# Performance work log

Hardware: AMD Instinct MI355X
Metric: run time of the kernel (lower is better)

Reference implementation:

```python
import jax, jax.numpy as jnp
import numpy as np

V, D, A = 100000, 128, 64
L, N, K = 3, 20000, 16


def setup_inputs() -> dict:
    key = jax.random.key(0)
    k1, k2, k3, k4, k5, k6 = jax.random.split(key, 6)
    Leaf_emb = jax.random.normal(k1, (V, D), dtype=jnp.float32)
    nodes = jax.random.randint(k2, (L, N), 0, V, dtype=jnp.int32)
    neighbors = jax.random.randint(k3, (L, N, K), 0, V, dtype=jnp.int32)
    masks = jnp.zeros((L, N, K), dtype=jnp.float32)  # additive mask, 0 = valid
    weights = jax.random.normal(k4, (L, N, K), dtype=jnp.float32)
    W_att = jax.random.uniform(k5, (2 * D, A), dtype=jnp.float32)
    b_att = jnp.zeros((A,), dtype=jnp.float32)
    v_att = jax.random.uniform(k6, (A,), dtype=jnp.float32)
    return {"Leaf_emb": Leaf_emb, "nodes": nodes, "neighbors": neighbors,
            "masks": masks, "weights": weights,
            "W_att": W_att, "b_att": b_att, "v_att": v_att}


def reference(Leaf_emb, nodes, neighbors, masks, weights, W_att, b_att, v_att):
    # Sequential over L tree levels (fixed, small): each level gathers node and
    # neighbor embeddings, scores neighbors with a 2-layer attention MLP,
    # combines masked-softmax attention with softmax'd structural weights,
    # sums neighbor embeddings and scatters the result back into W_tmp.
    W_tmp = Leaf_emb
    n_levels = nodes.shape[0]
    for i in range(n_levels):
        node = nodes[i]                      # [N] (constant across K in original)
        neighbor = neighbors[i]              # [N, K]
        mask = masks[i]                      # [N, K] additive
        weight = weights[i]                  # [N, K]
        node_tmp = Leaf_emb[node][:, None, :]          # [N, 1, D] from ORIGINAL emb
        neighbor_tmp = W_tmp[neighbor]                 # [N, K, D] from running emb
        node_b = jnp.broadcast_to(node_tmp, neighbor_tmp.shape)
        att_in = jnp.concatenate([node_b, neighbor_tmp], axis=2)  # [N, K, 2D]
        mlp = jax.nn.leaky_relu(att_in @ W_att + b_att, 0.01)     # [N, K, A]
        pre = mlp @ v_att                                         # [N, K]
        att = jax.nn.softmax(pre + mask, axis=1) * jax.nn.softmax(weight, axis=1)
        temp_emb = jnp.einsum('nkd,nk->nd', neighbor_tmp, att)    # [N, D]
        W_tmp = W_tmp.at[node].set(temp_emb)
    return W_tmp
```

## Files before the change

### kernel.cpp

```cpp
#include <hip/hip_runtime.h>
#include <math.h>

#define V 100000
#define D 128
#define A 64
#define LVLS 3
#define NN 20000
#define KK 16
#define BK2 16
#define AST2 18
#define BST2 68
#define PSTRIDE 128

__global__ __launch_bounds__(256, 4)
void projall_kernel(const float* __restrict__ Leaf, const float* __restrict__ Watt,
                    const float* __restrict__ batt, float* __restrict__ projAll,
                    float* __restrict__ outp) {
    __shared__ float As[128 * AST2];
    __shared__ float Bs[BK2 * BST2];
    int t = threadIdx.x;
    int tx = t & 15, ty = t >> 4;
    int r0 = blockIdx.x * 128;
    int half = blockIdx.y;
    const float* Wmat = Watt + (size_t)half * D * A;

    int ar = t >> 2;
    int ak = (t & 3) << 2;
    const float* asrc[2];
    int arow[2];
#pragma unroll
    for (int jj = 0; jj < 2; ++jj) {
        int r = r0 + ar + 64 * jj;
        arow[jj] = r;
        int rr = r < V ? r : V - 1;
        asrc[jj] = Leaf + (size_t)rr * D + ak;
    }
    int bk = t >> 4;
    int bc = (t & 15) << 2;

    float4 bv = make_float4(0.f, 0.f, 0.f, 0.f);
    if (half == 0) bv = *(const float4*)(batt + 4 * tx);
    float acc[8][4];
#pragma unroll
    for (int i = 0; i < 8; ++i) {
        acc[i][0] = bv.x; acc[i][1] = bv.y; acc[i][2] = bv.z; acc[i][3] = bv.w;
    }

    float4 pa0 = *(const float4*)(asrc[0]);
    float4 pa1 = *(const float4*)(asrc[1]);
    float4 pb  = *(const float4*)(Wmat + (size_t)bk * A + bc);

    for (int k0 = 0; k0 < D; k0 += BK2) {
        if (k0) __syncthreads();
        *(float4*)&As[(ar +  0) * AST2 + ak] = pa0;
        *(float4*)&As[(ar + 64) * AST2 + ak] = pa1;
        *(float4*)&Bs[bk * BST2 + bc] = pb;
        if (half == 0) {
            if (arow[0] < V) *(float4*)(outp + (size_t)arow[0] * D + k0 + ak) = pa0;
            if (arow[1] < V) *(float4*)(outp + (size_t)arow[1] * D + k0 + ak) = pa1;
        }
        __syncthreads();
        int kn = k0 + BK2;
        if (kn < D) {
            pa0 = *(const float4*)(asrc[0] + kn);
            pa1 = *(const float4*)(asrc[1] + kn);
            pb  = *(const float4*)(Wmat + (size_t)(kn + bk) * A + bc);
        }
#pragma unroll
        for (int kc = 0; kc < BK2; kc += 4) {
            float4 b0 = *(const float4*)&Bs[(kc + 0) * BST2 + 4 * tx];
            float4 b1 = *(const float4*)&Bs[(kc + 1) * BST2 + 4 * tx];
            float4 b2 = *(const float4*)&Bs[(kc + 2) * BST2 + 4 * tx];
            float4 b3 = *(const float4*)&Bs[(kc + 3) * BST2 + 4 * tx];
#pragma unroll
            for (int i = 0; i < 8; ++i) {
                float4 a = *(const float4*)&As[(8 * ty + i) * AST2 + kc];
                acc[i][0] = fmaf(a.x, b0.x, acc[i][0]);
                acc[i][0] = fmaf(a.y, b1.x, acc[i][0]);
                acc[i][0] = fmaf(a.z, b2.x, acc[i][0]);
                acc[i][0] = fmaf(a.w, b3.x, acc[i][0]);
                acc[i][1] = fmaf(a.x, b0.y, acc[i][1]);
                acc[i][1] = fmaf(a.y, b1.y, acc[i][1]);
                acc[i][1] = fmaf(a.z, b2.y, acc[i][1]);
                acc[i][1] = fmaf(a.w, b3.y, acc[i][1]);
                acc[i][2] = fmaf(a.x, b0.z, acc[i][2]);
                acc[i][2] = fmaf(a.y, b1.z, acc[i][2]);
                acc[i][2] = fmaf(a.z, b2.z, acc[i][2]);
                acc[i][2] = fmaf(a.w, b3.z, acc[i][2]);
                acc[i][3] = fmaf(a.x, b0.w, acc[i][3]);
                acc[i][3] = fmaf(a.y, b1.w, acc[i][3]);
                acc[i][3] = fmaf(a.z, b2.w, acc[i][3]);
                acc[i][3] = fmaf(a.w, b3.w, acc[i][3]);
            }
        }
    }

#pragma unroll
    for (int i = 0; i < 8; ++i) {
        int gr = r0 + 8 * ty + i;
        if (gr < V) {
            float4 o = make_float4(acc[i][0], acc[i][1], acc[i][2], acc[i][3]);
            *(float4*)(projAll + (size_t)gr * PSTRIDE + half * 64 + 4 * tx) = o;
        }
    }
}

__global__ __launch_bounds__(256, 4)
void commit_kernel(const float* __restrict__ tmp, const float* __restrict__ Wmat,
                   const int* __restrict__ nodes_l, const int* __restrict__ claim,
                   float* __restrict__ outp, float* __restrict__ projAll, int do_proj) {
    __shared__ float As[64 * AST2];
    __shared__ float Bs[BK2 * BST2];
    int t = threadIdx.x;
    int tx = t & 15, ty = t >> 4;
    int r0 = blockIdx.x * 64;

    int ar = t >> 2;
    int ak = (t & 3) << 2;
    int r = r0 + ar;
    int rr = r < NN ? r : NN - 1;
    const float* asrc = tmp + (size_t)rr * D + ak;
    int vrow = nodes_l[rr];
    int win = (r < NN) && (claim[vrow] == rr);

    int bk = t >> 4;
    int bc = (t & 15) << 2;

    float acc[4][4];
#pragma unroll
    for (int i = 0; i < 4; ++i) {
        acc[i][0] = 0.f; acc[i][1] = 0.f; acc[i][2] = 0.f; acc[i][3] = 0.f;
    }

    float4 pa = *(const float4*)(asrc);
    float4 pb = make_float4(0.f, 0.f, 0.f, 0.f);
    if (do_proj) pb = *(const float4*)(Wmat + (size_t)bk * A + bc);

    for (int k0 = 0; k0 < D; k0 += BK2) {
        if (k0) __syncthreads();
        *(float4*)&As[ar * AST2 + ak] = pa;
        if (do_proj) *(float4*)&Bs[bk * BST2 + bc] = pb;
        if (win)
            *(float4*)(outp + (size_t)vrow * D + k0 + ak) = pa;
        __syncthreads();
        int kn = k0 + BK2;
        if (kn < D) {
            pa = *(const float4*)(asrc + kn);
            if (do_proj) pb = *(const float4*)(Wmat + (size_t)(kn + bk) * A + bc);
        }
        if (do_proj) {
#pragma unroll
            for (int kc = 0; kc < BK2; kc += 4) {
                float4 b0 = *(const float4*)&Bs[(kc + 0) * BST2 + 4 * tx];
                float4 b1 = *(const float4*)&Bs[(kc + 1) * BST2 + 4 * tx];
                float4 b2 = *(const float4*)&Bs[(kc + 2) * BST2 + 4 * tx];
                float4 b3 = *(const float4*)&Bs[(kc + 3) * BST2 + 4 * tx];
#pragma unroll
                for (int i = 0; i < 4; ++i) {
                    float4 a = *(const float4*)&As[(4 * ty + i) * AST2 + kc];
                    acc[i][0] = fmaf(a.x, b0.x, acc[i][0]);
                    acc[i][0] = fmaf(a.y, b1.x, acc[i][0]);
                    acc[i][0] = fmaf(a.z, b2.x, acc[i][0]);
                    acc[i][0] = fmaf(a.w, b3.x, acc[i][0]);
                    acc[i][1] = fmaf(a.x, b0.y, acc[i][1]);
                    acc[i][1] = fmaf(a.y, b1.y, acc[i][1]);
                    acc[i][1] = fmaf(a.z, b2.y, acc[i][1]);
                    acc[i][1] = fmaf(a.w, b3.y, acc[i][1]);
                    acc[i][2] = fmaf(a.x, b0.z, acc[i][2]);
                    acc[i][2] = fmaf(a.y, b1.z, acc[i][2]);
                    acc[i][2] = fmaf(a.z, b2.z, acc[i][2]);
                    acc[i][2] = fmaf(a.w, b3.z, acc[i][2]);
                    acc[i][3] = fmaf(a.x, b0.w, acc[i][3]);
                    acc[i][3] = fmaf(a.y, b1.w, acc[i][3]);
                    acc[i][3] = fmaf(a.z, b2.w, acc[i][3]);
                    acc[i][3] = fmaf(a.w, b3.w, acc[i][3]);
                }
            }
        }
    }

    if (do_proj) {
#pragma unroll
        for (int i = 0; i < 4; ++i) {
            int gr = r0 + 4 * ty + i;
            if (gr < NN) {
                int v = nodes_l[gr];
                if (claim[v] == gr) {
                    float4 o = make_float4(acc[i][0], acc[i][1], acc[i][2], acc[i][3]);
                    *(float4*)(projAll + (size_t)v * PSTRIDE + 64 + 4 * tx) = o;
                }
            }
        }
    }
}

__global__ __launch_bounds__(256)
void attn_kernel(const float* __restrict__ Wc, const float* __restrict__ projAll,
                 const int* __restrict__ nodes_l, const int* __restrict__ neigh,
                 const float* __restrict__ maskp, const float* __restrict__ weightp,
                 const float* __restrict__ v_att, float* __restrict__ tmp) {
    int lane = threadIdx.x & 63;
    int n = blockIdx.x * 4 + (threadIdx.x >> 6);
    int k16 = lane & 15, q = lane >> 4;

    int   vnode = nodes_l[n];
    int   nbk = neigh[n * KK + k16];
    float wv  = weightp[n * KK + k16];
    float mk  = maskp[n * KK + k16];

    const float* npr = projAll + (size_t)vnode * PSTRIDE + q * 16;
    const float* var = v_att + q * 16;
    const float* pr  = projAll + (size_t)nbk * PSTRIDE + 64 + q * 16;

    float part = 0.f;
#pragma unroll
    for (int j = 0; j < 16; j += 4) {
        float4 npv = *(const float4*)(npr + j);
        float4 vav = *(const float4*)(var + j);
        float4 pv  = *(const float4*)(pr + j);
        float x;
        x = npv.x + pv.x; x = fmaxf(x, 0.01f * x); part = fmaf(x, vav.x, part);
        x = npv.y + pv.y; x = fmaxf(x, 0.01f * x); part = fmaf(x, vav.y, part);
        x = npv.z + pv.z; x = fmaxf(x, 0.01f * x); part = fmaf(x, vav.z, part);
        x = npv.w + pv.w; x = fmaxf(x, 0.01f * x); part = fmaf(x, vav.w, part);
    }
    part += __shfl_xor(part, 16);
    part += __shfl_xor(part, 32);
    float pre = part + mk;

    float mp = pre, mw = wv;
#pragma unroll
    for (int off = 8; off >= 1; off >>= 1) {
        mp = fmaxf(mp, __shfl_xor(mp, off));
        mw = fmaxf(mw, __shfl_xor(mw, off));
    }
    float ep = __expf(pre - mp), ew = __expf(wv - mw);
    float sp = ep, sw = ew;
#pragma unroll
    for (int off = 8; off >= 1; off >>= 1) {
        sp += __shfl_xor(sp, off);
        sw += __shfl_xor(sw, off);
    }
    float att = (ep / sp) * (ew / sw);

    int half = lane >> 5, li = lane & 31;
    float ax = 0.f, ay = 0.f, az = 0.f, aw = 0.f;
#pragma unroll
    for (int m = 0; m < 8; ++m) {
        int src = 2 * m + half;
        int nb   = __shfl(nbk, src);
        float ak = __shfl(att, src);
        float4 e = *(const float4*)&Wc[(size_t)nb * D + 4 * li];
        ax = fmaf(e.x, ak, ax); ay = fmaf(e.y, ak, ay);
        az = fmaf(e.z, ak, az); aw = fmaf(e.w, ak, aw);
    }
    ax += __shfl_xor(ax, 32); ay += __shfl_xor(ay, 32);
    az += __shfl_xor(az, 32); aw += __shfl_xor(aw, 32);
    if (half == 0) {
        float4 o = make_float4(ax, ay, az, aw);
        *(float4*)&tmp[(size_t)n * D + 4 * li] = o;
    }
}

__global__ void amax3_kernel(const int* __restrict__ nodes, int* __restrict__ claims, int total) {
    int i = blockIdx.x * 256 + threadIdx.x;
    if (i < total) {
        int lvl = i / NN, pos = i - lvl * NN;
        atomicMax(&claims[(size_t)lvl * V + nodes[i]], pos);
    }
}

extern "C" void kernel_launch(void* const* d_in, const int* in_sizes, int n_in,
                              void* d_out, int out_size, void* d_ws, size_t ws_size,
                              hipStream_t stream) {
    const float* Leaf    = (const float*)d_in[0];
    const int*   nodes   = (const int*)d_in[1];
    const int*   neigh   = (const int*)d_in[2];
    const float* masks   = (const float*)d_in[3];
    const float* weights = (const float*)d_in[4];
    const float* Watt    = (const float*)d_in[5];
    const float* batt    = (const float*)d_in[6];
    const float* vatt    = (const float*)d_in[7];
    float* out = (float*)d_out;

    char* ws = (char*)d_ws;
    float* projAll = (float*)ws;
    float* tmp     = (float*)(ws + (size_t)V * PSTRIDE * 4);
    int*   claims  = (int*)(ws + (size_t)(V * PSTRIDE + NN * D) * 4);

    hipMemsetAsync(claims, 0xFF, (size_t)LVLS * V * sizeof(int), stream);
    amax3_kernel<<<(LVLS * NN + 255) / 256, 256, 0, stream>>>(nodes, claims, LVLS * NN);
    projall_kernel<<<dim3((V + 127) / 128, 2), 256, 0, stream>>>(
        Leaf, Watt, batt, projAll, out);

    for (int l = 0; l < LVLS; ++l) {
        const int* nodes_l = nodes + l * NN;
        attn_kernel<<<NN / 4, 256, 0, stream>>>(out, projAll, nodes_l,
                                                neigh + (size_t)l * NN * KK,
                                                masks + (size_t)l * NN * KK,
                                                weights + (size_t)l * NN * KK, vatt, tmp);
        commit_kernel<<<(NN + 63) / 64, 256, 0, stream>>>(
            tmp, Watt + (size_t)D * A, nodes_l, claims + (size_t)l * V, out, projAll,
            (l + 1 < LVLS) ? 1 : 0);
    }
}
```

Measured before the change: 305.3 us.

## Merge projall halves into one block computing both W_att projections per row tile

Each block of the projection kernel now computes both the node-half and neighbor-half projections for its 128 rows, replacing the two-block grid dimension. Leaf rows are read from global memory once instead of twice, and the K-tile grows from 16 to 32. Each thread doubles its accumulators, which raises register pressure, and launch bounds drop to 3 blocks per CU to allow for that.

```diff
diff --git a/kernel.cpp b/kernel.cpp
--- a/kernel.cpp
+++ b/kernel.cpp
@@ -10,87 +10,116 @@
 #define BK2 16
 #define AST2 18
 #define BST2 68
+#define BK3 32
+#define AST3 34
+#define BST3 132
 #define PSTRIDE 128
 
-__global__ __launch_bounds__(256, 4)
+__global__ __launch_bounds__(256, 3)
 void projall_kernel(const float* __restrict__ Leaf, const float* __restrict__ Watt,
                     const float* __restrict__ batt, float* __restrict__ projAll,
                     float* __restrict__ outp) {
-    __shared__ float As[128 * AST2];
-    __shared__ float Bs[BK2 * BST2];
+    __shared__ float As[128 * AST3];
+    __shared__ float Bs[BK3 * BST3];
     int t = threadIdx.x;
     int tx = t & 15, ty = t >> 4;
     int r0 = blockIdx.x * 128;
-    int half = blockIdx.y;
-    const float* Wmat = Watt + (size_t)half * D * A;
-
-    int ar = t >> 2;
-    int ak = (t & 3) << 2;
-    const float* asrc[2];
-    int arow[2];
-#pragma unroll
-    for (int jj = 0; jj < 2; ++jj) {
-        int r = r0 + ar + 64 * jj;
+
+    int ar = t >> 3;
+    int ak = (t & 7) << 2;
+    const float* asrc[4];
+    int arow[4];
+#pragma unroll
+    for (int jj = 0; jj < 4; ++jj) {
+        int r = r0 + ar + 32 * jj;
         arow[jj] = r;
         int rr = r < V ? r : V - 1;
         asrc[jj] = Leaf + (size_t)rr * D + ak;
     }
-    int bk = t >> 4;
-    int bc = (t & 15) << 2;
-
-    float4 bv = make_float4(0.f, 0.f, 0.f, 0.f);
-    if (half == 0) bv = *(const float4*)(batt + 4 * tx);
-    float acc[8][4];
+    int bc = (t & 31) << 2;
+    int bk0 = t >> 5;
+    const float* bbase = (bc < 64) ? (Watt + bc) : (Watt + 128 * A + (bc - 64));
+
+    float4 bv = *(const float4*)(batt + 4 * tx);
+    float accA[8][4], accB[8][4];
 #pragma unroll
     for (int i = 0; i < 8; ++i) {
-        acc[i][0] = bv.x; acc[i][1] = bv.y; acc[i][2] = bv.z; acc[i][3] = bv.w;
-    }
-
-    float4 pa0 = *(const float4*)(asrc[0]);
-    float4 pa1 = *(const float4*)(asrc[1]);
-    float4 pb  = *(const float4*)(Wmat + (size_t)bk * A + bc);
-
-    for (int k0 = 0; k0 < D; k0 += BK2) {
+        accA[i][0] = bv.x; accA[i][1] = bv.y; accA[i][2] = bv.z; accA[i][3] = bv.w;
+        accB[i][0] = 0.f;  accB[i][1] = 0.f;  accB[i][2] = 0.f;  accB[i][3] = 0.f;
+    }
+
+    float4 pa[4], pb[4];
+#pragma unroll
+    for (int jj = 0; jj < 4; ++jj) pa[jj] = *(const float4*)(asrc[jj]);
+#pragma unroll
+    for (int ss = 0; ss < 4; ++ss)
+        pb[ss] = *(const float4*)(bbase + (size_t)(bk0 + 8 * ss) * A);
+
+    for (int k0 = 0; k0 < D; k0 += BK3) {
         if (k0) __syncthreads();
-        *(float4*)&As[(ar +  0) * AST2 + ak] = pa0;
-        *(float4*)&As[(ar + 64) * AST2 + ak] = pa1;
-        *(float4*)&Bs[bk * BST2 + bc] = pb;
-        if (half == 0) {
-            if (arow[0] < V) *(float4*)(outp + (size_t)arow[0] * D + k0 + ak) = pa0;
-            if (arow[1] < V) *(float4*)(outp + (size_t)arow[1] * D + k0 + ak) = pa1;
-        }
+#pragma unroll
+        for (int jj = 0; jj < 4; ++jj) {
+            *(float4*)&As[(ar + 32 * jj) * AST3 + ak] = pa[jj];
+            if (arow[jj] < V)
+                *(float4*)(outp + (size_t)arow[jj] * D + k0 + ak) = pa[jj];
+        }
+#pragma unroll
+        for (int ss = 0; ss < 4; ++ss)
+            *(float4*)&Bs[(bk0 + 8 * ss) * BST3 + bc] = pb[ss];
         __syncthreads();
-        int kn = k0 + BK2;
+        int kn = k0 + BK3;
         if (kn < D) {
-            pa0 = *(const float4*)(asrc[0] + kn);
-            pa1 = *(const float4*)(asrc[1] + kn);
-            pb  = *(const float4*)(Wmat + (size_t)(kn + bk) * A + bc);
-        }
-#pragma unroll
-        for (int kc = 0; kc < BK2; kc += 4) {
-            float4 b0 = *(const float4*)&Bs[(kc + 0) * BST2 + 4 * tx];
-            float4 b1 = *(const float4*)&Bs[(kc + 1) * BST2 + 4 * tx];
-            float4 b2 = *(const float4*)&Bs[(kc + 2) * BST2 + 4 * tx];
-            float4 b3 = *(const float4*)&Bs[(kc + 3) * BST2 + 4 * tx];
+#pragma unroll
+            for (int jj = 0; jj < 4; ++jj) pa[jj] = *(const float4*)(asrc[jj] + kn);
+#pragma unroll
+            for (int ss = 0; ss < 4; ++ss)
+                pb[ss] = *(const float4*)(bbase + (size_t)(kn + bk0 + 8 * ss) * A);
+        }
+#pragma unroll
+        for (int kc = 0; kc < BK3; kc += 4) {
+            float4 a0 = *(const float4*)&Bs[(kc + 0) * BST3 + 4 * tx];
+            float4 a1 = *(const float4*)&Bs[(kc + 1) * BST3 + 4 * tx];
+            float4 a2 = *(const float4*)&Bs[(kc + 2) * BST3 + 4 * tx];
+            float4 a3 = *(const float4*)&Bs[(kc + 3) * BST3 + 4 * tx];
+            float4 c0 = *(const float4*)&Bs[(kc + 0) * BST3 + 64 + 4 * tx];
+            float4 c1 = *(const float4*)&Bs[(kc + 1) * BST3 + 64 + 4 * tx];
+            float4 c2 = *(const float4*)&Bs[(kc + 2) * BST3 + 64 + 4 * tx];
+            float4 c3 = *(const float4*)&Bs[(kc + 3) * BST3 + 64 + 4 * tx];
 #pragma unroll
             for (int i = 0; i < 8; ++i) {
-                float4 a = *(const float4*)&As[(8 * ty + i) * AST2 + kc];
-                acc[i][0] = fmaf(a.x, b0.x, acc[i][0]);
-                acc[i][0] = fmaf(a.y, b1.x, acc[i][0]);
-                acc[i][0] = fmaf(a.z, b2.x, acc[i][0]);
-                acc[i][0] = fmaf(a.w, b3.x, acc[i][0]);
-                acc[i][1] = fmaf(a.x, b0.y, acc[i][1]);
-                acc[i][1] = fmaf(a.y, b1.y, acc[i][1]);
-                acc[i][1] = fmaf(a.z, b2.y, acc[i][1]);
-                acc[i][1] = fmaf(a.w, b3.y, acc[i][1]);
-                acc[i][2] = fmaf(a.x, b0.z, acc[i][2]);
-                acc[i][2] = fmaf(a.y, b1.z, acc[i][2]);
-                acc[i][2] = fmaf(a.z, b2.z, acc[i][2]);
-                acc[i][2] = fmaf(a.w, b3.z, acc[i][2]);
-                acc[i][3] = fmaf(a.x, b0.w, acc[i][3]);
-                acc[i][3] = fmaf(a.y, b1.w, acc[i][3]);
-                acc[i][3] = fmaf(a.z, b2.w, acc[i][3]);
-                acc[i][3] = fmaf(a.w, b3.w, acc[i][3]);
+                float4 a = *(const float4*)&As[(8 * ty + i) * AST3 + kc];
+                accA[i][0] = fmaf(a.x, a0.x, accA[i][0]);
+                accA[i][0] = fmaf(a.y, a1.x, accA[i][0]);
+                accA[i][0] = fmaf(a.z, a2.x, accA[i][0]);
+                accA[i][0] = fmaf(a.w, a3.x, accA[i][0]);
+                accA[i][1] = fmaf(a.x, a0.y, accA[i][1]);
+                accA[i][1] = fmaf(a.y, a1.y, accA[i][1]);
+                accA[i][1] = fmaf(a.z, a2.y, accA[i][1]);
+                accA[i][1] = fmaf(a.w, a3.y, accA[i][1]);
+                accA[i][2] = fmaf(a.x, a0.z, accA[i][2]);
+                accA[i][2] = fmaf(a.y, a1.z, accA[i][2]);
+                accA[i][2] = fmaf(a.z, a2.z, accA[i][2]);
+                accA[i][2] = fmaf(a.w, a3.z, accA[i][2]);
+                accA[i][3] = fmaf(a.x, a0.w, accA[i][3]);
+                accA[i][3] = fmaf(a.y, a1.w, accA[i][3]);
+                accA[i][3] = fmaf(a.z, a2.w, accA[i][3]);
+                accA[i][3] = fmaf(a.w, a3.w, accA[i][3]);
+                accB[i][0] = fmaf(a.x, c0.x, accB[i][0]);
+                accB[i][0] = fmaf(a.y, c1.x, accB[i][0]);
+                accB[i][0] = fmaf(a.z, c2.x, accB[i][0]);
+                accB[i][0] = fmaf(a.w, c3.x, accB[i][0]);
+                accB[i][1] = fmaf(a.x, c0.y, accB[i][1]);
+                accB[i][1] = fmaf(a.y, c1.y, accB[i][1]);
+                accB[i][1] = fmaf(a.z, c2.y, accB[i][1]);
+                accB[i][1] = fmaf(a.w, c3.y, accB[i][1]);
+                accB[i][2] = fmaf(a.x, c0.z, accB[i][2]);
+                accB[i][2] = fmaf(a.y, c1.z, accB[i][2]);
+                accB[i][2] = fmaf(a.z, c2.z, accB[i][2]);
+                accB[i][2] = fmaf(a.w, c3.z, accB[i][2]);
+                accB[i][3] = fmaf(a.x, c0.w, accB[i][3]);
+                accB[i][3] = fmaf(a.y, c1.w, accB[i][3]);
+                accB[i][3] = fmaf(a.z, c2.w, accB[i][3]);
+                accB[i][3] = fmaf(a.w, c3.w, accB[i][3]);
             }
         }
     }
@@ -99,8 +128,10 @@
     for (int i = 0; i < 8; ++i) {
         int gr = r0 + 8 * ty + i;
         if (gr < V) {
-            float4 o = make_float4(acc[i][0], acc[i][1], acc[i][2], acc[i][3]);
-            *(float4*)(projAll + (size_t)gr * PSTRIDE + half * 64 + 4 * tx) = o;
+            float4 oA = make_float4(accA[i][0], accA[i][1], accA[i][2], accA[i][3]);
+            float4 oB = make_float4(accB[i][0], accB[i][1], accB[i][2], accB[i][3]);
+            *(float4*)(projAll + (size_t)gr * PSTRIDE + 4 * tx) = oA;
+            *(float4*)(projAll + (size_t)gr * PSTRIDE + 64 + 4 * tx) = oB;
         }
     }
 }
@@ -290,8 +321,7 @@
 
     hipMemsetAsync(claims, 0xFF, (size_t)LVLS * V * sizeof(int), stream);
     amax3_kernel<<<(LVLS * NN + 255) / 256, 256, 0, stream>>>(nodes, claims, LVLS * NN);
-    projall_kernel<<<dim3((V + 127) / 128, 2), 256, 0, stream>>>(
-        Leaf, Watt, batt, projAll, out);
+    projall_kernel<<<(V + 127) / 128, 256, 0, stream>>>(Leaf, Watt, batt, projAll, out);
 
     for (int l = 0; l < LVLS; ++l) {
         const int* nodes_l = nodes + l * NN;
```

New measurement: 397.9 us. 1.3x slower.
